# Performance work log

Hardware: AMD Instinct MI355X
Metric: run time of the kernel (lower is better)

Reference implementation:

```python
import jax, jax.numpy as jnp
import numpy as np
from jax.scipy.linalg import solve_triangular

N = 512      # latent_dim
K = 64       # k_spa
D = 16       # n_domains
B = 1024     # batch

# strictly-lower-triangular entries in the last K rows, row-major (matches torch code order)
_L_IDX = np.array(sum([[(i, j) for j in range(i)] for i in range(N - K, N)], []), dtype=np.int32)
_S_IDX = np.arange(N - K, N, dtype=np.int32)   # last K diagonal entries
N_L = _L_IDX.shape[0]


def setup_inputs() -> dict:
    key = jax.random.key(0)
    k_eps, k_d, k_L, k_S, k_bn, k_bs = jax.random.split(key, 6)
    return {
        "epsilon": jax.random.normal(k_eps, (B, N), dtype=jnp.float32),
        "d": jax.random.randint(k_d, (B,), 0, D, dtype=jnp.int32),
        # learned parameters (decode path): embedding tables + biases
        "L_emb": jax.random.normal(k_L, (D, N_L), dtype=jnp.float32) * 0.1,
        "S_emb": jax.random.normal(k_S, (D, K), dtype=jnp.float32),
        "bias_nonshared": jax.random.normal(k_bn, (D, K), dtype=jnp.float32),
        "bias_shared": jax.random.normal(k_bs, (N - K,), dtype=jnp.float32),
    }


def reference(epsilon, d, L_emb, S_emb, bias_nonshared, bias_shared):
    # --- build per-domain L (strictly lower triangular, zero for domain 0) ---
    L = jnp.zeros((D, N, N), dtype=epsilon.dtype)
    L = L.at[1:, _L_IDX[:, 0], _L_IDX[:, 1]].set(L_emb[1:])          # [D, N, N]

    # --- build per-domain S (diagonal, identity for domain 0) ---
    ar = jnp.arange(N)
    S = jnp.zeros((D, N, N), dtype=epsilon.dtype).at[:, ar, ar].set(1.0)
    S = S.at[1:, _S_IDX, _S_IDX].set(S_emb[1:])                      # [D, N, N]

    # --- F_d = (I - L_d)^{-1} S_d ; I - L_d is unit lower triangular -> forward substitution ---
    A = jnp.eye(N, dtype=epsilon.dtype) - L                          # [D, N, N]
    F_ds = solve_triangular(A, S, lower=True)                        # [D, N, N]

    # --- embedding gather + batched matvec ---
    F_b = F_ds[d]                                                    # [B, N, N]
    z = jnp.einsum('bij,bj->bi', F_b, epsilon)                       # [B, N]

    bias = jnp.concatenate(
        [jnp.broadcast_to(bias_shared, (epsilon.shape[0], N - K)), bias_nonshared[d]],
        axis=-1,
    )
    return z + bias
```

## Files before the change

### kernel.cpp

```cpp
#include <hip/hip_runtime.h>

#define NTOT 512
#define NH   448
#define KK   64
#define NL   30688
#define DD   16

__global__ __launch_bounds__(256)
void fvae_fused(const float* __restrict__ eps,
                const int*   __restrict__ dom_idx,
                const float* __restrict__ L_emb,
                const float* __restrict__ S_emb,
                const float* __restrict__ bias_ns,
                const float* __restrict__ bias_sh,
                float*       __restrict__ out)
{
    const int b    = blockIdx.x;
    const int tid  = threadIdx.x;
    const int wave = tid >> 6;
    const int lane = tid & 63;

    __shared__ float y_s[KK];
    __shared__ float U_s[(KK * (KK - 1)) / 2];

    const int dom = dom_idx[b];
    const float* __restrict__ epsb = eps + (size_t)b * NTOT;
    float*       __restrict__ outb = out + (size_t)b * NTOT;

    if (dom == 0) {
        if (tid < 128) {
            const float4 e = *(const float4*)(epsb + tid * 4);
            float4 bv;
            if (tid < 112) bv = *(const float4*)(bias_sh + tid * 4);
            else           bv = *(const float4*)(bias_ns + (tid - 112) * 4);
            float4 o; o.x = e.x + bv.x; o.y = e.y + bv.y;
            o.z = e.z + bv.z; o.w = e.w + bv.w;
            *(float4*)(outb + tid * 4) = o;
        }
        return;
    }

    const float* __restrict__ Ld = L_emb + (size_t)dom * NL;

    float er[7];
    #pragma unroll
    for (int k = 0; k < 7; ++k) er[k] = epsb[lane + 64 * k];

    if (wave == 0) {
        for (int q = lane; q < NH / 4; q += 64) {
            const float4 e  = *(const float4*)(epsb + q * 4);
            const float4 bs = *(const float4*)(bias_sh + q * 4);
            float4 o; o.x = e.x + bs.x; o.y = e.y + bs.y;
            o.z = e.z + bs.z; o.w = e.w + bs.w;
            *(float4*)(outb + q * 4) = o;
        }
    } else {
        for (int r = wave; r < KK; r += 3)
            if (lane < r)
                U_s[(r * (r - 1)) / 2 + lane] =
                    Ld[r * NH + (r * (r - 1)) / 2 + NH + lane];
    }
    __syncthreads();

    #pragma unroll
    for (int bt = 0; bt < 4; ++bt) {
        const int r0 = wave * 16 + bt * 4;
        float a0, a1, a2, a3;
        {
            const float* __restrict__ T0 = Ld + (r0    ) * NH + ((r0    ) * (r0 - 1)) / 2;
            const float* __restrict__ T1 = Ld + (r0 + 1) * NH + ((r0 + 1) * (r0    )) / 2;
            const float* __restrict__ T2 = Ld + (r0 + 2) * NH + ((r0 + 2) * (r0 + 1)) / 2;
            const float* __restrict__ T3 = Ld + (r0 + 3) * NH + ((r0 + 3) * (r0 + 2)) / 2;
            a0 = T0[lane]*er[0] + T0[lane+64]*er[1] + T0[lane+128]*er[2]
               + T0[lane+192]*er[3] + T0[lane+256]*er[4] + T0[lane+320]*er[5]
               + T0[lane+384]*er[6];
            a1 = T1[lane]*er[0] + T1[lane+64]*er[1] + T1[lane+128]*er[2]
               + T1[lane+192]*er[3] + T1[lane+256]*er[4] + T1[lane+320]*er[5]
               + T1[lane+384]*er[6];
            a2 = T2[lane]*er[0] + T2[lane+64]*er[1] + T2[lane+128]*er[2]
               + T2[lane+192]*er[3] + T2[lane+256]*er[4] + T2[lane+320]*er[5]
               + T2[lane+384]*er[6];
            a3 = T3[lane]*er[0] + T3[lane+64]*er[1] + T3[lane+128]*er[2]
               + T3[lane+192]*er[3] + T3[lane+256]*er[4] + T3[lane+320]*er[5]
               + T3[lane+384]*er[6];
        }
        a0 += __shfl_xor(a0, 1);  a1 += __shfl_xor(a1, 1);
        a2 += __shfl_xor(a2, 1);  a3 += __shfl_xor(a3, 1);
        float c0 = (lane & 1) ? a1 : a0;
        float c1 = (lane & 1) ? a3 : a2;
        c0 += __shfl_xor(c0, 2);  c1 += __shfl_xor(c1, 2);
        float dsum = (lane & 2) ? c1 : c0;
        dsum += __shfl_xor(dsum, 4);
        dsum += __shfl_xor(dsum, 8);
        dsum += __shfl_xor(dsum, 16);
        dsum += __shfl_xor(dsum, 32);
        if (lane < 4) {
            const int r = r0 + lane;
            y_s[r] = dsum + S_emb[dom * KK + r] * epsb[NH + r];
        }
    }
    __syncthreads();

    if (wave == 0) {
        const int m  = lane;
        const int tb = (m * (m - 1)) / 2;
        float z = y_s[m];
        #pragma unroll
        for (int r = 0; r < KK - 1; ++r) {
            const float u = (r < m) ? U_s[tb + r] : 0.f;
            z += u * __shfl(z, r);
        }
        outb[NH + m] = z + bias_ns[dom * KK + m];
    }
}

extern "C" void kernel_launch(void* const* d_in, const int* in_sizes, int n_in,
                              void* d_out, int out_size, void* d_ws, size_t ws_size,
                              hipStream_t stream) {
    const float* eps     = (const float*)d_in[0];
    const int*   dom     = (const int*)  d_in[1];
    const float* L_emb   = (const float*)d_in[2];
    const float* S_emb   = (const float*)d_in[3];
    const float* bias_ns = (const float*)d_in[4];
    const float* bias_sh = (const float*)d_in[5];
    float* out = (float*)d_out;

    const int B = in_sizes[0] / NTOT;
    fvae_fused<<<dim3(B), dim3(256), 0, stream>>>(eps, dom, L_emb, S_emb,
                                                  bias_ns, bias_sh, out);
}
```

Before: 17.29 us.

## Repack L embeddings into aligned dense workspace for vectorized float4 loads

Adds a pre-pass kernel that copies each domain's L_emb into an aligned, padded layout in the workspace. It stores the 448-column rectangular block densely and the 64x64 triangular block zero-padded. The main kernel then reads both with float4 loads, and eps with float4 loads too, in place of scalar, unaligned triangular-offset accesses. The shared triangle becomes a padded 2D array. This costs an extra kernel launch and a write/read round trip through the workspace on every call, in exchange for wider, aligned memory accesses.

```diff
diff --git a/kernel.cpp b/kernel.cpp
--- a/kernel.cpp
+++ b/kernel.cpp
@@ -6,10 +6,38 @@
 #define NL   30688
 #define DD   16
 
+#define TP_STRIDE 28672
+#define UPOFF     (DD * TP_STRIDE)
+#define UP_STRIDE 4096
+
+
+__global__ __launch_bounds__(256)
+void fvae_repack(const float* __restrict__ L_emb, float* __restrict__ ws)
+{
+    const int dom  = blockIdx.x >> 3;
+    const int part = blockIdx.x & 7;
+    const int tid  = threadIdx.x;
+    if (dom == 0) return;
+
+    const float* __restrict__ Ld = L_emb + (size_t)dom * NL;
+    float* __restrict__ Tp = ws + (size_t)dom * TP_STRIDE;
+    float* __restrict__ Up = ws + UPOFF + (size_t)dom * UP_STRIDE;
+
+    for (int i = part * 3584 + tid; i < (part + 1) * 3584 + (part == 7 ? 0 : 0); i += 256) {
+        const int r = i / 448;
+        Tp[i] = Ld[i + (r * (r - 1)) / 2];
+    }
+
+    for (int i = part * 512 + tid; i < (part + 1) * 512; i += 256) {
+        const int r = i >> 6, m = i & 63;
+        Up[i] = (m < r) ? Ld[r * NH + (r * (r - 1)) / 2 + NH + m] : 0.f;
+    }
+}
+
 __global__ __launch_bounds__(256)
 void fvae_fused(const float* __restrict__ eps,
                 const int*   __restrict__ dom_idx,
-                const float* __restrict__ L_emb,
+                const float* __restrict__ ws,
                 const float* __restrict__ S_emb,
                 const float* __restrict__ bias_ns,
                 const float* __restrict__ bias_sh,
@@ -21,7 +49,7 @@
     const int lane = tid & 63;
 
     __shared__ float y_s[KK];
-    __shared__ float U_s[(KK * (KK - 1)) / 2];
+    __shared__ float U_s[KK][KK + 1];
 
     const int dom = dom_idx[b];
     const float* __restrict__ epsb = eps + (size_t)b * NTOT;
@@ -40,11 +68,12 @@
         return;
     }
 
-    const float* __restrict__ Ld = L_emb + (size_t)dom * NL;
+    const float* __restrict__ Tp = ws + (size_t)dom * TP_STRIDE;
+    const float* __restrict__ Up = ws + UPOFF + (size_t)dom * UP_STRIDE;
 
-    float er[7];
-    #pragma unroll
-    for (int k = 0; k < 7; ++k) er[k] = epsb[lane + 64 * k];
+    const float4 ea = *(const float4*)(epsb + lane * 4);
+    float4 eb = make_float4(0.f, 0.f, 0.f, 0.f);
+    if (lane < 48) eb = *(const float4*)(epsb + 256 + lane * 4);
 
     if (wave == 0) {
         for (int q = lane; q < NH / 4; q += 64) {
@@ -55,10 +84,13 @@
             *(float4*)(outb + q * 4) = o;
         }
     } else {
-        for (int r = wave; r < KK; r += 3)
-            if (lane < r)
-                U_s[(r * (r - 1)) / 2 + lane] =
-                    Ld[r * NH + (r * (r - 1)) / 2 + NH + lane];
+        const int t2 = tid - 64;
+        for (int i = t2; i < 1024; i += 192) {
+            const float4 v = *(const float4*)(Up + i * 4);
+            const int r = i >> 4, m = (i & 15) * 4;
+            U_s[r][m] = v.x; U_s[r][m + 1] = v.y;
+            U_s[r][m + 2] = v.z; U_s[r][m + 3] = v.w;
+        }
     }
     __syncthreads();
 
@@ -67,22 +99,23 @@
         const int r0 = wave * 16 + bt * 4;
         float a0, a1, a2, a3;
         {
-            const float* __restrict__ T0 = Ld + (r0    ) * NH + ((r0    ) * (r0 - 1)) / 2;
-            const float* __restrict__ T1 = Ld + (r0 + 1) * NH + ((r0 + 1) * (r0    )) / 2;
-            const float* __restrict__ T2 = Ld + (r0 + 2) * NH + ((r0 + 2) * (r0 + 1)) / 2;
-            const float* __restrict__ T3 = Ld + (r0 + 3) * NH + ((r0 + 3) * (r0 + 2)) / 2;
-            a0 = T0[lane]*er[0] + T0[lane+64]*er[1] + T0[lane+128]*er[2]
-               + T0[lane+192]*er[3] + T0[lane+256]*er[4] + T0[lane+320]*er[5]
-               + T0[lane+384]*er[6];
-            a1 = T1[lane]*er[0] + T1[lane+64]*er[1] + T1[lane+128]*er[2]
-               + T1[lane+192]*er[3] + T1[lane+256]*er[4] + T1[lane+320]*er[5]
-               + T1[lane+384]*er[6];
-            a2 = T2[lane]*er[0] + T2[lane+64]*er[1] + T2[lane+128]*er[2]
-               + T2[lane+192]*er[3] + T2[lane+256]*er[4] + T2[lane+320]*er[5]
-               + T2[lane+384]*er[6];
-            a3 = T3[lane]*er[0] + T3[lane+64]*er[1] + T3[lane+128]*er[2]
-               + T3[lane+192]*er[3] + T3[lane+256]*er[4] + T3[lane+320]*er[5]
-               + T3[lane+384]*er[6];
+            const float4* __restrict__ T0 = (const float4*)(Tp + (r0    ) * 448);
+            const float4* __restrict__ T1 = (const float4*)(Tp + (r0 + 1) * 448);
+            const float4* __restrict__ T2 = (const float4*)(Tp + (r0 + 2) * 448);
+            const float4* __restrict__ T3 = (const float4*)(Tp + (r0 + 3) * 448);
+            const float4 p0 = T0[lane], p1 = T1[lane], p2 = T2[lane], p3 = T3[lane];
+            a0 = p0.x*ea.x + p0.y*ea.y + p0.z*ea.z + p0.w*ea.w;
+            a1 = p1.x*ea.x + p1.y*ea.y + p1.z*ea.z + p1.w*ea.w;
+            a2 = p2.x*ea.x + p2.y*ea.y + p2.z*ea.z + p2.w*ea.w;
+            a3 = p3.x*ea.x + p3.y*ea.y + p3.z*ea.z + p3.w*ea.w;
+            if (lane < 48) {
+                const float4 q0 = T0[64 + lane], q1 = T1[64 + lane],
+                             q2 = T2[64 + lane], q3 = T3[64 + lane];
+                a0 += q0.x*eb.x + q0.y*eb.y + q0.z*eb.z + q0.w*eb.w;
+                a1 += q1.x*eb.x + q1.y*eb.y + q1.z*eb.z + q1.w*eb.w;
+                a2 += q2.x*eb.x + q2.y*eb.y + q2.z*eb.z + q2.w*eb.w;
+                a3 += q3.x*eb.x + q3.y*eb.y + q3.z*eb.z + q3.w*eb.w;
+            }
         }
         a0 += __shfl_xor(a0, 1);  a1 += __shfl_xor(a1, 1);
         a2 += __shfl_xor(a2, 1);  a3 += __shfl_xor(a3, 1);
@@ -102,12 +135,11 @@
     __syncthreads();
 
     if (wave == 0) {
-        const int m  = lane;
-        const int tb = (m * (m - 1)) / 2;
+        const int m = lane;
         float z = y_s[m];
         #pragma unroll
         for (int r = 0; r < KK - 1; ++r) {
-            const float u = (r < m) ? U_s[tb + r] : 0.f;
+            const float u = (r < m) ? U_s[m][r] : 0.f;
             z += u * __shfl(z, r);
         }
         outb[NH + m] = z + bias_ns[dom * KK + m];
@@ -124,8 +156,10 @@
     const float* bias_ns = (const float*)d_in[4];
     const float* bias_sh = (const float*)d_in[5];
     float* out = (float*)d_out;
+    float* ws  = (float*)d_ws;
 
     const int B = in_sizes[0] / NTOT;
-    fvae_fused<<<dim3(B), dim3(256), 0, stream>>>(eps, dom, L_emb, S_emb,
-                                                  bias_ns, bias_sh, out);
+    fvae_repack<<<dim3(DD * 8), dim3(256), 0, stream>>>(L_emb, ws);
+    fvae_fused <<<dim3(B),      dim3(256), 0, stream>>>(eps, dom, ws, S_emb,
+                                                        bias_ns, bias_sh, out);
 }
```

Result: slower. 21.85 us (+26.4%).

## Group batch rows by domain and process two rows per block to reuse L

Applied to the files above, without the earlier changes.

The launch changes from one block per batch row to a grid of 16 domains × 32 slices. Each block scans all domain indices with a wave ballot and builds a list of the rows that belong to its domain and slice. It then processes those rows two at a time, so every L-row load from memory serves two dot products, which roughly halves L-embedding traffic. In exchange, every block pays for a scan of the full index array, the batch size is hardcoded to 1024, and the load per block depends on how the domains are distributed.

```diff
diff --git a/kernel.cpp b/kernel.cpp
--- a/kernel.cpp
+++ b/kernel.cpp
@@ -5,6 +5,9 @@
 #define KK   64
 #define NL   30688
 #define DD   16
+#define BB   1024
+#define SLICES 32
+#define SLCAP  32
 
 __global__ __launch_bounds__(256)
 void fvae_fused(const float* __restrict__ eps,
@@ -15,46 +18,36 @@
                 const float* __restrict__ bias_sh,
                 float*       __restrict__ out)
 {
-    const int b    = blockIdx.x;
-    const int tid  = threadIdx.x;
-    const int wave = tid >> 6;
-    const int lane = tid & 63;
+    const int dom   = blockIdx.x & 15;
+    const int slice = blockIdx.x >> 4;
+    const int tid   = threadIdx.x;
+    const int wave  = tid >> 6;
+    const int lane  = tid & 63;
 
-    __shared__ float y_s[KK];
+    __shared__ int   list_s[SLCAP];
+    __shared__ int   gt_s;
+    __shared__ float y_s[2][KK];
     __shared__ float U_s[(KK * (KK - 1)) / 2];
-
-    const int dom = dom_idx[b];
-    const float* __restrict__ epsb = eps + (size_t)b * NTOT;
-    float*       __restrict__ outb = out + (size_t)b * NTOT;
-
-    if (dom == 0) {
-        if (tid < 128) {
-            const float4 e = *(const float4*)(epsb + tid * 4);
-            float4 bv;
-            if (tid < 112) bv = *(const float4*)(bias_sh + tid * 4);
-            else           bv = *(const float4*)(bias_ns + (tid - 112) * 4);
-            float4 o; o.x = e.x + bv.x; o.y = e.y + bv.y;
-            o.z = e.z + bv.z; o.w = e.w + bv.w;
-            *(float4*)(outb + tid * 4) = o;
-        }
-        return;
-    }
 
     const float* __restrict__ Ld = L_emb + (size_t)dom * NL;
 
-    float er[7];
-    #pragma unroll
-    for (int k = 0; k < 7; ++k) er[k] = epsb[lane + 64 * k];
-
     if (wave == 0) {
-        for (int q = lane; q < NH / 4; q += 64) {
-            const float4 e  = *(const float4*)(epsb + q * 4);
-            const float4 bs = *(const float4*)(bias_sh + q * 4);
-            float4 o; o.x = e.x + bs.x; o.y = e.y + bs.y;
-            o.z = e.z + bs.z; o.w = e.w + bs.w;
-            *(float4*)(outb + q * 4) = o;
+        int dm[BB / 64];
+        #pragma unroll
+        for (int t = 0; t < BB / 64; ++t) dm[t] = dom_idx[t * 64 + lane];
+        int base = 0;
+        #pragma unroll
+        for (int t = 0; t < BB / 64; ++t) {
+            const unsigned long long mt = __ballot(dm[t] == dom);
+            if (dm[t] == dom) {
+                const int rank = base + __popcll(mt & ((1ull << lane) - 1ull));
+                if ((rank & (SLICES - 1)) == slice) list_s[rank >> 5] = t * 64 + lane;
+            }
+            base += __popcll(mt);
         }
-    } else {
+        if (lane == 0)
+            gt_s = (base > slice) ? (base - 1 - slice) / SLICES + 1 : 0;
+    } else if (dom != 0) {
         for (int r = wave; r < KK; r += 3)
             if (lane < r)
                 U_s[(r * (r - 1)) / 2 + lane] =
@@ -62,55 +55,107 @@
     }
     __syncthreads();
 
-    #pragma unroll
-    for (int bt = 0; bt < 4; ++bt) {
-        const int r0 = wave * 16 + bt * 4;
-        float a0, a1, a2, a3;
-        {
+    const int G_total = gt_s;
+    if (G_total == 0) return;
+
+    for (int s0 = 0; s0 < G_total; s0 += 2) {
+        const int i0 = list_s[s0];
+        const int i1 = list_s[(s0 + 1 < G_total) ? s0 + 1 : s0];
+        const float* __restrict__ e0 = eps + (size_t)i0 * NTOT;
+        const float* __restrict__ e1 = eps + (size_t)i1 * NTOT;
+        float*       __restrict__ o0 = out + (size_t)i0 * NTOT;
+        float*       __restrict__ o1 = out + (size_t)i1 * NTOT;
+
+        if (dom == 0) {
+            const int g = tid >> 7, q = tid & 127;
+            const float* __restrict__ eb = g ? e1 : e0;
+            float*       __restrict__ ob = g ? o1 : o0;
+            const float4 e = *(const float4*)(eb + q * 4);
+            float4 bv;
+            if (q < 112) bv = *(const float4*)(bias_sh + q * 4);
+            else         bv = *(const float4*)(bias_ns + (q - 112) * 4);
+            float4 o; o.x = e.x + bv.x; o.y = e.y + bv.y;
+            o.z = e.z + bv.z; o.w = e.w + bv.w;
+            *(float4*)(ob + q * 4) = o;
+            continue;
+        }
+
+        if (tid < 2 * (NH / 4)) {
+            const int g = tid / 112, q = tid - g * 112;
+            const float* __restrict__ eb = g ? e1 : e0;
+            float*       __restrict__ ob = g ? o1 : o0;
+            const float4 e  = *(const float4*)(eb + q * 4);
+            const float4 bs = *(const float4*)(bias_sh + q * 4);
+            float4 o; o.x = e.x + bs.x; o.y = e.y + bs.y;
+            o.z = e.z + bs.z; o.w = e.w + bs.w;
+            *(float4*)(ob + q * 4) = o;
+        }
+
+        float er0[7], er1[7];
+        #pragma unroll
+        for (int k = 0; k < 7; ++k) er0[k] = e0[lane + 64 * k];
+        #pragma unroll
+        for (int k = 0; k < 7; ++k) er1[k] = e1[lane + 64 * k];
+
+        #pragma unroll
+        for (int bt = 0; bt < 4; ++bt) {
+            const int r0 = wave * 16 + bt * 4;
             const float* __restrict__ T0 = Ld + (r0    ) * NH + ((r0    ) * (r0 - 1)) / 2;
             const float* __restrict__ T1 = Ld + (r0 + 1) * NH + ((r0 + 1) * (r0    )) / 2;
             const float* __restrict__ T2 = Ld + (r0 + 2) * NH + ((r0 + 2) * (r0 + 1)) / 2;
             const float* __restrict__ T3 = Ld + (r0 + 3) * NH + ((r0 + 3) * (r0 + 2)) / 2;
-            a0 = T0[lane]*er[0] + T0[lane+64]*er[1] + T0[lane+128]*er[2]
-               + T0[lane+192]*er[3] + T0[lane+256]*er[4] + T0[lane+320]*er[5]
-               + T0[lane+384]*er[6];
-            a1 = T1[lane]*er[0] + T1[lane+64]*er[1] + T1[lane+128]*er[2]
-               + T1[lane+192]*er[3] + T1[lane+256]*er[4] + T1[lane+320]*er[5]
-               + T1[lane+384]*er[6];
-            a2 = T2[lane]*er[0] + T2[lane+64]*er[1] + T2[lane+128]*er[2]
-               + T2[lane+192]*er[3] + T2[lane+256]*er[4] + T2[lane+320]*er[5]
-               + T2[lane+384]*er[6];
-            a3 = T3[lane]*er[0] + T3[lane+64]*er[1] + T3[lane+128]*er[2]
-               + T3[lane+192]*er[3] + T3[lane+256]*er[4] + T3[lane+320]*er[5]
-               + T3[lane+384]*er[6];
+            float a00 = 0.f, a01 = 0.f, a02 = 0.f, a03 = 0.f;
+            float a10 = 0.f, a11 = 0.f, a12 = 0.f, a13 = 0.f;
+            #pragma unroll
+            for (int k = 0; k < 7; ++k) {
+                const float t0 = T0[lane + 64 * k], t1 = T1[lane + 64 * k],
+                            t2 = T2[lane + 64 * k], t3 = T3[lane + 64 * k];
+                a00 += t0 * er0[k]; a01 += t1 * er0[k];
+                a02 += t2 * er0[k]; a03 += t3 * er0[k];
+                a10 += t0 * er1[k]; a11 += t1 * er1[k];
+                a12 += t2 * er1[k]; a13 += t3 * er1[k];
+            }
+            a00 += __shfl_xor(a00, 1);  a01 += __shfl_xor(a01, 1);
+            a02 += __shfl_xor(a02, 1);  a03 += __shfl_xor(a03, 1);
+            float c00 = (lane & 1) ? a01 : a00;
+            float c01 = (lane & 1) ? a03 : a02;
+            c00 += __shfl_xor(c00, 2);  c01 += __shfl_xor(c01, 2);
+            float d0 = (lane & 2) ? c01 : c00;
+            d0 += __shfl_xor(d0, 4);  d0 += __shfl_xor(d0, 8);
+            d0 += __shfl_xor(d0, 16); d0 += __shfl_xor(d0, 32);
+
+            a10 += __shfl_xor(a10, 1);  a11 += __shfl_xor(a11, 1);
+            a12 += __shfl_xor(a12, 1);  a13 += __shfl_xor(a13, 1);
+            float c10 = (lane & 1) ? a11 : a10;
+            float c11 = (lane & 1) ? a13 : a12;
+            c10 += __shfl_xor(c10, 2);  c11 += __shfl_xor(c11, 2);
+            float d1 = (lane & 2) ? c11 : c10;
+            d1 += __shfl_xor(d1, 4);  d1 += __shfl_xor(d1, 8);
+            d1 += __shfl_xor(d1, 16); d1 += __shfl_xor(d1, 32);
+
+            if (lane < 4) {
+                const int r = r0 + lane;
+                const float sr = S_emb[dom * KK + r];
+                y_s[0][r] = d0 + sr * e0[NH + r];
+                y_s[1][r] = d1 + sr * e1[NH + r];
+            }
         }
-        a0 += __shfl_xor(a0, 1);  a1 += __shfl_xor(a1, 1);
-        a2 += __shfl_xor(a2, 1);  a3 += __shfl_xor(a3, 1);
-        float c0 = (lane & 1) ? a1 : a0;
-        float c1 = (lane & 1) ? a3 : a2;
-        c0 += __shfl_xor(c0, 2);  c1 += __shfl_xor(c1, 2);
-        float dsum = (lane & 2) ? c1 : c0;
-        dsum += __shfl_xor(dsum, 4);
-        dsum += __shfl_xor(dsum, 8);
-        dsum += __shfl_xor(dsum, 16);
-        dsum += __shfl_xor(dsum, 32);
-        if (lane < 4) {
-            const int r = r0 + lane;
-            y_s[r] = dsum + S_emb[dom * KK + r] * epsb[NH + r];
+        __syncthreads();
+
+        if (wave < 2) {
+            const float* __restrict__ eb = wave ? e1 : e0; (void)eb;
+            float*       __restrict__ ob = wave ? o1 : o0;
+            const int m  = lane;
+            const int tb = (m * (m - 1)) / 2;
+            float z = y_s[wave][m];
+            #pragma unroll
+            for (int r = 0; r < KK - 1; ++r) {
+                const float u = (r < m) ? U_s[tb + r] : 0.f;
+                z += u * __shfl(z, r);
+            }
+            ob[NH + m] = z + bias_ns[dom * KK + m];
         }
-    }
-    __syncthreads();
-
-    if (wave == 0) {
-        const int m  = lane;
-        const int tb = (m * (m - 1)) / 2;
-        float z = y_s[m];
-        #pragma unroll
-        for (int r = 0; r < KK - 1; ++r) {
-            const float u = (r < m) ? U_s[tb + r] : 0.f;
-            z += u * __shfl(z, r);
-        }
-        outb[NH + m] = z + bias_ns[dom * KK + m];
+        if (s0 + 2 < G_total) __syncthreads();
     }
 }
 
@@ -125,7 +170,6 @@
     const float* bias_sh = (const float*)d_in[5];
     float* out = (float*)d_out;
 
-    const int B = in_sizes[0] / NTOT;
-    fvae_fused<<<dim3(B), dim3(256), 0, stream>>>(eps, dom, L_emb, S_emb,
-                                                  bias_ns, bias_sh, out);
+    fvae_fused<<<dim3(DD * SLICES), dim3(256), 0, stream>>>(
+        eps, dom, L_emb, S_emb, bias_ns, bias_sh, out);
 }
```

Result: slower. 22.65 us (+31.0%).

## Double block size to 512 threads and stage epsilon in shared memory

Applied to the files above, without the earlier changes.

Launches 512 threads per batch row instead of 256, so each of 8 waves reduces 8 rows of L instead of 16. Epsilon is loaded once into shared memory and reused for the bias-add output, register staging and the diagonal term, replacing repeated global loads. The U triangle copy is spread over 7 waves. The aim is more memory-level parallelism per row, at the cost of more threads per block, idle threads in domain-0 blocks, and an extra barrier-dependent shared-memory stage.

```diff
diff --git a/kernel.cpp b/kernel.cpp
--- a/kernel.cpp
+++ b/kernel.cpp
@@ -6,7 +6,7 @@
 #define NL   30688
 #define DD   16
 
-__global__ __launch_bounds__(256)
+__global__ __launch_bounds__(512, 8)
 void fvae_fused(const float* __restrict__ eps,
                 const int*   __restrict__ dom_idx,
                 const float* __restrict__ L_emb,
@@ -20,6 +20,7 @@
     const int wave = tid >> 6;
     const int lane = tid & 63;
 
+    __shared__ float eps_s[NTOT];
     __shared__ float y_s[KK];
     __shared__ float U_s[(KK * (KK - 1)) / 2];
 
@@ -42,61 +43,50 @@
 
     const float* __restrict__ Ld = L_emb + (size_t)dom * NL;
 
-    float er[7];
-    #pragma unroll
-    for (int k = 0; k < 7; ++k) er[k] = epsb[lane + 64 * k];
+    eps_s[tid] = epsb[tid];
 
-    if (wave == 0) {
-        for (int q = lane; q < NH / 4; q += 64) {
-            const float4 e  = *(const float4*)(epsb + q * 4);
-            const float4 bs = *(const float4*)(bias_sh + q * 4);
-            float4 o; o.x = e.x + bs.x; o.y = e.y + bs.y;
-            o.z = e.z + bs.z; o.w = e.w + bs.w;
-            *(float4*)(outb + q * 4) = o;
-        }
-    } else {
-        for (int r = wave; r < KK; r += 3)
+    if (wave != 0) {
+        for (int r = wave; r < KK; r += 7)
             if (lane < r)
                 U_s[(r * (r - 1)) / 2 + lane] =
                     Ld[r * NH + (r * (r - 1)) / 2 + NH + lane];
     }
     __syncthreads();
 
+    if (tid < NH / 4) {
+        const float4 e  = *(const float4*)&eps_s[tid * 4];
+        const float4 bs = *(const float4*)(bias_sh + tid * 4);
+        float4 o; o.x = e.x + bs.x; o.y = e.y + bs.y;
+        o.z = e.z + bs.z; o.w = e.w + bs.w;
+        *(float4*)(outb + tid * 4) = o;
+    }
+
+    float er[7];
+    #pragma unroll
+    for (int k = 0; k < 7; ++k) er[k] = eps_s[lane + 64 * k];
+
     #pragma unroll
     for (int bt = 0; bt < 4; ++bt) {
-        const int r0 = wave * 16 + bt * 4;
-        float a0, a1, a2, a3;
-        {
-            const float* __restrict__ T0 = Ld + (r0    ) * NH + ((r0    ) * (r0 - 1)) / 2;
-            const float* __restrict__ T1 = Ld + (r0 + 1) * NH + ((r0 + 1) * (r0    )) / 2;
-            const float* __restrict__ T2 = Ld + (r0 + 2) * NH + ((r0 + 2) * (r0 + 1)) / 2;
-            const float* __restrict__ T3 = Ld + (r0 + 3) * NH + ((r0 + 3) * (r0 + 2)) / 2;
-            a0 = T0[lane]*er[0] + T0[lane+64]*er[1] + T0[lane+128]*er[2]
-               + T0[lane+192]*er[3] + T0[lane+256]*er[4] + T0[lane+320]*er[5]
-               + T0[lane+384]*er[6];
-            a1 = T1[lane]*er[0] + T1[lane+64]*er[1] + T1[lane+128]*er[2]
-               + T1[lane+192]*er[3] + T1[lane+256]*er[4] + T1[lane+320]*er[5]
-               + T1[lane+384]*er[6];
-            a2 = T2[lane]*er[0] + T2[lane+64]*er[1] + T2[lane+128]*er[2]
-               + T2[lane+192]*er[3] + T2[lane+256]*er[4] + T2[lane+320]*er[5]
-               + T2[lane+384]*er[6];
-            a3 = T3[lane]*er[0] + T3[lane+64]*er[1] + T3[lane+128]*er[2]
-               + T3[lane+192]*er[3] + T3[lane+256]*er[4] + T3[lane+320]*er[5]
-               + T3[lane+384]*er[6];
-        }
-        a0 += __shfl_xor(a0, 1);  a1 += __shfl_xor(a1, 1);
-        a2 += __shfl_xor(a2, 1);  a3 += __shfl_xor(a3, 1);
-        float c0 = (lane & 1) ? a1 : a0;
-        float c1 = (lane & 1) ? a3 : a2;
-        c0 += __shfl_xor(c0, 2);  c1 += __shfl_xor(c1, 2);
-        float dsum = (lane & 2) ? c1 : c0;
-        dsum += __shfl_xor(dsum, 4);
-        dsum += __shfl_xor(dsum, 8);
-        dsum += __shfl_xor(dsum, 16);
-        dsum += __shfl_xor(dsum, 32);
-        if (lane < 4) {
+        const int r0 = wave * 8 + bt * 2;
+        const float* __restrict__ T0 = Ld + (r0    ) * NH + ((r0    ) * (r0 - 1)) / 2;
+        const float* __restrict__ T1 = Ld + (r0 + 1) * NH + ((r0 + 1) * (r0    )) / 2;
+        float a0 = T0[lane]*er[0] + T0[lane+64]*er[1] + T0[lane+128]*er[2]
+                 + T0[lane+192]*er[3] + T0[lane+256]*er[4] + T0[lane+320]*er[5]
+                 + T0[lane+384]*er[6];
+        float a1 = T1[lane]*er[0] + T1[lane+64]*er[1] + T1[lane+128]*er[2]
+                 + T1[lane+192]*er[3] + T1[lane+256]*er[4] + T1[lane+320]*er[5]
+                 + T1[lane+384]*er[6];
+        a0 += __shfl_xor(a0, 1);
+        a1 += __shfl_xor(a1, 1);
+        float c = (lane & 1) ? a1 : a0;
+        c += __shfl_xor(c, 2);
+        c += __shfl_xor(c, 4);
+        c += __shfl_xor(c, 8);
+        c += __shfl_xor(c, 16);
+        c += __shfl_xor(c, 32);
+        if (lane < 2) {
             const int r = r0 + lane;
-            y_s[r] = dsum + S_emb[dom * KK + r] * epsb[NH + r];
+            y_s[r] = c + S_emb[dom * KK + r] * eps_s[NH + r];
         }
     }
     __syncthreads();
@@ -126,6 +116,6 @@
     float* out = (float*)d_out;
 
     const int B = in_sizes[0] / NTOT;
-    fvae_fused<<<dim3(B), dim3(256), 0, stream>>>(eps, dom, L_emb, S_emb,
+    fvae_fused<<<dim3(B), dim3(512), 0, stream>>>(eps, dom, L_emb, S_emb,
                                                   bias_ns, bias_sh, out);
 }
```

Result: faster. 15.47 us (-10.5%).
